# Kernel tuning notes

Hardware: AMD Instinct MI355X
Metric: run time of the kernel (lower is better)

## Reference

```python
import jax, jax.numpy as jnp
import numpy as np
from jax import lax

D_MODEL = 1024
D_STATE = 128
HEADDIM = 64
EXPAND = 2
NGROUPS = 1
CHUNK = 256
D_INNER = EXPAND * D_MODEL          # 2048
D_SSM = D_INNER                      # d_ssm defaults to d_inner
NHEADS = D_SSM // HEADDIM            # 32
CONV_DIM = D_SSM + 2 * NGROUPS * D_STATE   # 2304
D_IN_PROJ = 2 * D_INNER + 2 * NGROUPS * D_STATE + NHEADS  # 4384 -> d_mlp = 0
BATCH = 2
SEQLEN = 2048
EPS = 1e-5


def setup_inputs() -> dict:
    key = jax.random.key(0)
    ks = jax.random.split(key, 9)
    u = jax.random.normal(ks[0], (BATCH, SEQLEN, D_MODEL), jnp.float32)
    # indices into left-padded (len = SEQLEN+1) sequence; 0 selects the zero pad
    conv_indices = jax.random.randint(ks[1], (BATCH, 4 * SEQLEN), 0, SEQLEN + 1)
    W_in = jax.random.normal(ks[2], (D_IN_PROJ, D_MODEL), jnp.float32) / np.sqrt(D_MODEL).astype(np.float32)
    conv_w = jax.random.normal(ks[3], (CONV_DIM, 4), jnp.float32) * 0.2
    conv_b = jax.random.normal(ks[4], (CONV_DIM,), jnp.float32) * 0.02
    # dt_bias init exactly as the module: inverse-softplus of dt in [dt_min, dt_max]
    dt = jnp.exp(jax.random.uniform(ks[5], (NHEADS,), jnp.float32) * (np.log(0.1) - np.log(0.001)) + np.log(0.001))
    dt = jnp.clip(dt, 1e-4)
    dt_bias = dt + jnp.log(-jnp.expm1(-dt))
    A_log = jnp.log(jax.random.uniform(ks[6], (NHEADS,), jnp.float32, minval=1.0, maxval=16.0))
    D = jnp.ones((NHEADS,), jnp.float32)
    norm_w = jnp.ones((D_SSM,), jnp.float32)
    W_out = jax.random.normal(ks[7], (D_MODEL, D_INNER), jnp.float32) / np.sqrt(D_INNER).astype(np.float32)
    return dict(u=u, conv_indices=conv_indices, W_in=W_in, conv_w=conv_w, conv_b=conv_b,
                dt_bias=dt_bias, A_log=A_log, D=D, norm_w=norm_w, W_out=W_out)


def _segsum(x):
    # x: (b, c, h, cs) -> (b, c, h, cs, cs); out[..., t, s] = sum_{k=s+1..t} x[..., k]
    cs = x.shape[-1]
    cx = jnp.cumsum(x, axis=-1)
    diff = cx[..., :, None] - cx[..., None, :]
    mask = jnp.tril(jnp.ones((cs, cs), dtype=bool))
    return jnp.where(mask, diff, -jnp.inf)


def _ssd(x, dt, A, Bh, Ch, D):
    # Mamba2 SSD chunked scan. x:(b,l,h,p), dt:(b,l,h), A:(h,), Bh/Ch:(b,l,h,n), D:(h,)
    b, l, h, p = x.shape
    n = Bh.shape[-1]
    c = l // CHUNK
    xr = x.reshape(b, c, CHUNK, h, p)
    dtr = dt.reshape(b, c, CHUNK, h)
    Br = Bh.reshape(b, c, CHUNK, h, n)
    Cr = Ch.reshape(b, c, CHUNK, h, n)
    dA = dtr * A                                 # (b,c,cs,h)
    Acum = jnp.cumsum(dA, axis=2)                # (b,c,cs,h)
    Lm = jnp.exp(_segsum(jnp.transpose(dA, (0, 1, 3, 2))))  # (b,c,h,cs,cs)
    dtx = xr * dtr[..., None]                    # dt-weighted inputs
    # intra-chunk (diagonal blocks)
    Yd = jnp.einsum('bcthn,bcshn,bchts,bcshp->bcthp', Cr, Br, Lm, dtx)
    # per-chunk final states
    decay_states = jnp.exp(Acum[:, :, -1:, :] - Acum)        # (b,c,cs,h)
    states = jnp.einsum('bcshn,bcsh,bcshp->bchpn', Br, decay_states, dtx)
    chunk_decay = jnp.exp(Acum[:, :, -1, :])     # (b,c,h)
    def step(h_prev, inp):
        dec, st = inp
        return h_prev * dec[..., None, None] + st, h_prev
    init = jnp.zeros((b, h, p, n), x.dtype)
    _, prev = lax.scan(step, init, (jnp.moveaxis(chunk_decay, 1, 0), jnp.moveaxis(states, 1, 0)))
    prev = jnp.moveaxis(prev, 0, 1)              # (b,c,h,p,n): state entering each chunk
    # inter-chunk (off-diagonal) contribution
    Yoff = jnp.einsum('bcthn,bchpn,bcth->bcthp', Cr, prev, jnp.exp(Acum))
    Y = Yd + Yoff + D[None, None, None, :, None] * xr
    return Y.reshape(b, l, h, p)


def reference(u, conv_indices, W_in, conv_w, conv_b, dt_bias, A_log, D, norm_w, W_out):
    b, l, _ = u.shape
    zxbcdt = u @ W_in.T                          # (b,l,4384); d_mlp == 0
    z, xBC, dt_raw = jnp.split(zxbcdt, [D_SSM, D_SSM + CONV_DIM], axis=-1)
    # tree conv: left-pad seq by 1, gather 4 tree positions per output step, depthwise conv k=4 stride=4
    xc = jnp.transpose(xBC, (0, 2, 1))           # (b, conv_dim, l)
    xp = jnp.pad(xc, ((0, 0), (0, 0), (1, 0)))
    idx = jnp.broadcast_to(conv_indices[:, None, :], (b, CONV_DIM, 4 * l))
    g = jnp.take_along_axis(xp, idx, axis=2).reshape(b, CONV_DIM, l, 4)
    conv = jnp.einsum('bclk,ck->bcl', g, conv_w) + conv_b[None, :, None]
    xBC = jax.nn.silu(jnp.transpose(conv, (0, 2, 1)))  # (b,l,conv_dim)
    x, Bm, Cm = jnp.split(xBC, [D_SSM, D_SSM + NGROUPS * D_STATE], axis=-1)
    x = x.reshape(b, l, NHEADS, HEADDIM)
    hpg = NHEADS // NGROUPS
    Bh = jnp.repeat(Bm.reshape(b, l, NGROUPS, D_STATE), hpg, axis=2)
    Ch = jnp.repeat(Cm.reshape(b, l, NGROUPS, D_STATE), hpg, axis=2)
    dt = jax.nn.softplus(dt_raw + dt_bias)       # dt_softplus=True, default dt_limit
    A = -jnp.exp(A_log.astype(jnp.float32))
    y = _ssd(x, dt, A, Bh, Ch, D).reshape(b, l, D_SSM)
    # RMSNormGated, norm_before_gate=False, group_size = d_ssm (ngroups=1)
    yz = y * jax.nn.silu(z)
    var = jnp.mean(jnp.square(yz), axis=-1, keepdims=True)
    y = yz * lax.rsqrt(var + EPS) * norm_w
    return y @ W_out.T
```

## Files before the change

### kernel.cpp

```cpp
#include <hip/hip_runtime.h>

#define BB 2
#define LL 2048
#define DMODEL 1024
#define DSSM 2048
#define NH 32
#define HD 64
#define DST 128
#define CONVD 2304
#define DPROJ 4384
#define CS 64
#define NC 32
#define BLTOT (BB*LL)

typedef short v8s __attribute__((ext_vector_type(8)));
typedef float v4f __attribute__((ext_vector_type(4)));

__device__ __forceinline__ float b2f(unsigned short h) {
  union { unsigned int u; float f; } v; v.u = ((unsigned int)h) << 16; return v.f;
}
__device__ __forceinline__ unsigned short f2b(float f) {
  union { float f; unsigned int u; } v; v.f = f;
  unsigned int u = v.u;
  return (unsigned short)((u + 0x7fffu + ((u >> 16) & 1u)) >> 16);
}
__device__ __forceinline__ v4f mfma16(v8s a, v8s b, v4f c) {
  return __builtin_amdgcn_mfma_f32_16x16x32_bf16(a, b, c, 0, 0, 0);
}
__device__ __forceinline__ void gl_lds16(const unsigned short* g, unsigned short* l) {
  __builtin_amdgcn_global_load_lds(
      (const __attribute__((address_space(1))) void*)(g),
      (__attribute__((address_space(3))) void*)(l), 16, 0, 0);
}

__global__ __launch_bounds__(256) void cvt3_kernel(
    const float* __restrict__ a, unsigned short* __restrict__ oa, int na4,
    const float* __restrict__ b, unsigned short* __restrict__ ob, int nb4,
    const float* __restrict__ c, unsigned short* __restrict__ oc, int nc4)
{
  int i = blockIdx.x * 256 + threadIdx.x;
  const float* src; unsigned short* dst; int j;
  if (i < na4) { src = a; dst = oa; j = i; }
  else if (i < na4 + nb4) { src = b; dst = ob; j = i - na4; }
  else if (i < na4 + nb4 + nc4) { src = c; dst = oc; j = i - na4 - nb4; }
  else return;
  float4 v = ((const float4*)src)[j];
  ushort4 o;
  o.x = f2b(v.x); o.y = f2b(v.y); o.z = f2b(v.z); o.w = f2b(v.w);
  ((ushort4*)dst)[j] = o;
}

template<int TN, int OUT_BF16, int DBUF>
__global__ __launch_bounds__(256) void gemm_bt(
    const unsigned short* __restrict__ A, const unsigned short* __restrict__ Bt,
    void* __restrict__ Cout, int M, int N, int K, int ldc)
{
  constexpr int NT = TN / 32;
  constexpr int NB = DBUF ? 2 : 1;
  const int bm = blockIdx.x, bn = blockIdx.y;
  const int tid = threadIdx.x;
  const int wave = tid >> 6, lane = tid & 63;
  const int wm = wave & 1, wn = wave >> 1;
  const int q = lane >> 4, lr = lane & 15;

  __shared__ __align__(16) unsigned short As[NB][128 * 64];
  __shared__ __align__(16) unsigned short Bs[NB][TN * 64];

  v4f acc[4][NT];
#pragma unroll
  for (int i = 0; i < 4; i++)
#pragma unroll
    for (int j = 0; j < NT; j++) acc[i][j] = v4f{0.f, 0.f, 0.f, 0.f};

  const int lrow = lane >> 3;
  const int gchunk = (lane & 7) ^ lrow;

#define STAGE_TILE(bufi, k0) do {                                              \
    _Pragma("unroll")                                                          \
    for (int it = 0; it < 4; ++it) {                                           \
      int r = wave * 32 + it * 8 + lrow;                                       \
      gl_lds16(A + (size_t)(bm * 128 + r) * K + (k0) + gchunk * 8,             \
               &As[bufi][(wave * 32 + it * 8) * 64]);                          \
    }                                                                          \
    _Pragma("unroll")                                                          \
    for (int it = 0; it < TN / 32; ++it) {                                     \
      int rloc = wave * (TN / 4) + it * 8;                                     \
      int rb = bn * TN + rloc + lrow; if (rb >= N) rb = N - 1;                 \
      gl_lds16(Bt + (size_t)rb * K + (k0) + gchunk * 8, &Bs[bufi][rloc * 64]); \
    }                                                                          \
  } while (0)

#define COMPUTE_TILE(bufi) do {                                                \
    const unsigned short* __restrict__ Ab = As[bufi];                          \
    const unsigned short* __restrict__ Bb = Bs[bufi];                          \
    _Pragma("unroll")                                                          \
    for (int ks = 0; ks < 64; ks += 32) {                                      \
      const int c0 = (ks >> 3) + q;                                            \
      v8s af[4], bf[NT];                                                       \
      _Pragma("unroll")                                                        \
      for (int mt = 0; mt < 4; ++mt) {                                         \
        int r = wm * 64 + mt * 16 + lr;                                        \
        af[mt] = *(const v8s*)&Ab[r * 64 + ((c0 ^ (r & 7)) << 3)];             \
      }                                                                        \
      _Pragma("unroll")                                                        \
      for (int nt = 0; nt < NT; ++nt) {                                        \
        int r = wn * (TN / 2) + nt * 16 + lr;                                  \
        bf[nt] = *(const v8s*)&Bb[r * 64 + ((c0 ^ (r & 7)) << 3)];             \
      }                                                                        \
      _Pragma("unroll")                                                        \
      for (int mt = 0; mt < 4; ++mt)                                           \
        _Pragma("unroll")                                                      \
        for (int nt = 0; nt < NT; ++nt)                                        \
          acc[mt][nt] = mfma16(af[mt], bf[nt], acc[mt][nt]);                   \
    }                                                                          \
  } while (0)

#define WAIT_BARRIER() do {                                                    \
    __builtin_amdgcn_sched_barrier(0);                                         \
    asm volatile("s_waitcnt vmcnt(0) lgkmcnt(0)\ns_barrier" ::: "memory");     \
  } while (0)

  if constexpr (DBUF == 0) {
    for (int k0 = 0; k0 < K; k0 += 64) {
      __syncthreads();
      STAGE_TILE(0, k0);
      __syncthreads();
      COMPUTE_TILE(0);
    }
  } else {
    const int nkt = K >> 6;
    STAGE_TILE(0, 0);
    WAIT_BARRIER();
    for (int kt = 0; kt < nkt; ++kt) {
      const int cb = kt & 1;
      if (kt + 1 < nkt) STAGE_TILE(cb ^ 1, (kt + 1) << 6);
      COMPUTE_TILE(cb);
      if (kt + 1 < nkt) WAIT_BARRIER();
    }
  }
#undef STAGE_TILE
#undef COMPUTE_TILE
#undef WAIT_BARRIER

#pragma unroll
  for (int mt = 0; mt < 4; ++mt) {
#pragma unroll
    for (int nt = 0; nt < NT; ++nt) {
      int row = bm * 128 + wm * 64 + mt * 16 + q * 4;
      int col = bn * TN + wn * (TN / 2) + nt * 16 + lr;
      if (col < N) {
#pragma unroll
        for (int r = 0; r < 4; ++r) {
          float v = acc[mt][nt][r];
          if (OUT_BF16) ((unsigned short*)Cout)[(size_t)(row + r) * ldc + col] = f2b(v);
          else          ((float*)Cout)[(size_t)(row + r) * ldc + col] = v;
        }
      }
    }
  }
}

__global__ __launch_bounds__(256) void convBC_kernel(
    const unsigned short* __restrict__ C1, const int* __restrict__ cidx,
    const float* __restrict__ convw, const float* __restrict__ convb,
    const float* __restrict__ dtbias,
    unsigned short* __restrict__ Bg16, unsigned short* __restrict__ Cg16,
    unsigned short* __restrict__ BgT16, float* __restrict__ dtb)
{
  int bl0 = blockIdx.x * 16;
  int b = bl0 >> 11;
  int tid = threadIdx.x;
  __shared__ int idxs[64];
  if (tid < 64) {
    int tk = tid >> 2, k = tid & 3;
    idxs[tid] = cidx[b * (4 * LL) + (((bl0 + tk) & 2047) * 4) + k];
  }
  __syncthreads();
  const float4* cw4 = (const float4*)convw;
  int quad = tid & 63;
  int relc = DSSM + quad * 4;
  float4 w0 = cw4[relc], w1 = cw4[relc + 1], w2 = cw4[relc + 2], w3 = cw4[relc + 3];
  float4 cb = *(const float4*)(convb + relc);
  int tk0 = (tid >> 6) * 4;
  int cc = relc - DSSM;
  unsigned short btc[4][4];
#pragma unroll
  for (int tt = 0; tt < 4; ++tt) {
    int tk = tk0 + tt;
    int bl = bl0 + tk;
    ushort4 rv[4];
#pragma unroll
    for (int k = 0; k < 4; ++k) {
      int iv = idxs[tk * 4 + k];
      rv[k] = (iv > 0) ? *(const ushort4*)(C1 + (size_t)(b * LL + iv - 1) * DPROJ + DSSM + relc)
                       : make_ushort4(0, 0, 0, 0);
    }
    float a0 = cb.x + b2f(rv[0].x) * w0.x + b2f(rv[1].x) * w0.y + b2f(rv[2].x) * w0.z + b2f(rv[3].x) * w0.w;
    float a1 = cb.y + b2f(rv[0].y) * w1.x + b2f(rv[1].y) * w1.y + b2f(rv[2].y) * w1.z + b2f(rv[3].y) * w1.w;
    float a2 = cb.z + b2f(rv[0].z) * w2.x + b2f(rv[1].z) * w2.y + b2f(rv[2].z) * w2.z + b2f(rv[3].z) * w2.w;
    float a3 = cb.w + b2f(rv[0].w) * w3.x + b2f(rv[1].w) * w3.y + b2f(rv[2].w) * w3.z + b2f(rv[3].w) * w3.w;
    ushort4 o;
    o.x = f2b(a0 / (1.f + __expf(-a0)));
    o.y = f2b(a1 / (1.f + __expf(-a1)));
    o.z = f2b(a2 / (1.f + __expf(-a2)));
    o.w = f2b(a3 / (1.f + __expf(-a3)));
    if (cc < DST) {
      *(ushort4*)(Bg16 + (size_t)bl * DST + cc) = o;
      btc[0][tt] = o.x; btc[1][tt] = o.y; btc[2][tt] = o.z; btc[3][tt] = o.w;
    } else {
      *(ushort4*)(Cg16 + (size_t)bl * DST + (cc - DST)) = o;
    }
  }
  if (cc < DST) {
#pragma unroll
    for (int c = 0; c < 4; ++c)
      *(ushort4*)(BgT16 + (size_t)(cc + c) * BLTOT + bl0 + tk0) =
          make_ushort4(btc[c][0], btc[c][1], btc[c][2], btc[c][3]);
  }
  for (int u = tid; u < 16 * NH; u += 256) {
    int tk = u >> 5, hh = u & 31;
    int bl = bl0 + tk;
    float raw = b2f(C1[(size_t)bl * DPROJ + DSSM + CONVD + hh]) + dtbias[hh];
    float dtv = (raw > 20.f) ? raw : log1pf(__expf(raw));
    dtb[(size_t)bl * NH + hh] = dtv;
  }
}

__global__ __launch_bounds__(256) void d1_intra(
    const unsigned short* __restrict__ C1, const int* __restrict__ cidx,
    const float* __restrict__ convw, const float* __restrict__ convb,
    const unsigned short* __restrict__ Bg16,
    const unsigned short* __restrict__ Cg16,
    const unsigned short* __restrict__ BgT16, const float* __restrict__ dtb,
    const float* __restrict__ A_log, const float* __restrict__ Dp,
    unsigned short* __restrict__ y16, unsigned short* __restrict__ statesb,
    float* __restrict__ cdb, float* __restrict__ acumb)
{
  int gid = blockIdx.x;
  int h = gid & 31, ci = (gid >> 5) & 31, b = gid >> 10;
  int tid = threadIdx.x, wave = tid >> 6, lane = tid & 63, q = lane >> 4, lr = lane & 15;

  __shared__ __align__(16) unsigned short BnG[CS * 136];
  __shared__ __align__(16) unsigned short BTw[DST * 72];
  __shared__ __align__(16) unsigned short xT[HD * 72];
  __shared__ float dt_s[CS], ac_s[CS], dec_s[CS];
  __shared__ int idxs[CS * 4];
  __shared__ float wls[HD * 4];
  __shared__ float bls[HD];

  const size_t blbase = (size_t)b * LL + ci * CS;
  const size_t chbase = (size_t)(b * NC + ci) * NH + h;
  float Ah = -__expf(A_log[h]);

  if (wave == 0) {
    float d = dtb[(blbase + lane) * NH + h];
    float a = d * Ah;
#pragma unroll
    for (int off = 1; off < 64; off <<= 1) {
      float u = __shfl_up(a, off, 64);
      if (lane >= off) a += u;
    }
    float tot = __shfl(a, 63, 64);
    dt_s[lane] = d;
    ac_s[lane] = a;
    dec_s[lane] = __expf(tot - a);
    acumb[chbase * CS + lane] = a;
    if (lane == 0) cdb[chbase] = __expf(tot);
  }

#pragma unroll
  for (int g = 0; g < 8; ++g) {
    int f = g * 256 + tid;
    int s = f >> 5, c4 = (f & 31) * 4;
    *(ushort4*)&BnG[s * 136 + c4] = *(const ushort4*)(Bg16 + (blbase + s) * DST + c4);
  }
  {
    int s = tid >> 2, k = tid & 3;
    idxs[tid] = cidx[b * (4 * LL) + (ci * CS + s) * 4 + k];
  }
  if (tid < HD) *(float4*)&wls[tid * 4] = *(const float4*)(convw + (h * HD + tid) * 4);
  if (tid < HD / 4) *(float4*)&bls[tid * 4] = *(const float4*)(convb + h * HD + tid * 4);
  __syncthreads();

#pragma unroll
  for (int g = 0; g < 8; ++g) {
    int f = g * 256 + tid;
    int n = f >> 4, s4 = (f & 15) * 4;
    ushort4 bv = *(const ushort4*)(BgT16 + (size_t)n * BLTOT + blbase + s4);
    ushort4 o;
    o.x = f2b(b2f(bv.x) * dec_s[s4 + 0] * dt_s[s4 + 0]);
    o.y = f2b(b2f(bv.y) * dec_s[s4 + 1] * dt_s[s4 + 1]);
    o.z = f2b(b2f(bv.z) * dec_s[s4 + 2] * dt_s[s4 + 2]);
    o.w = f2b(b2f(bv.w) * dec_s[s4 + 3] * dt_s[s4 + 3]);
    *(ushort4*)&BTw[n * 72 + s4] = o;
  }

  v4f accS[4];
#pragma unroll
  for (int i = 0; i < 4; i++) accS[i] = v4f{0.f, 0.f, 0.f, 0.f};
#pragma unroll
  for (int ks = 0; ks < 128; ks += 32) {
    v8s a = *(const v8s*)(Cg16 + (blbase + wave * 16 + lr) * DST + ks + q * 8);
#pragma unroll
    for (int si = 0; si < 4; ++si) {
      v8s bb = *(const v8s*)&BnG[(si * 16 + lr) * 136 + ks + q * 8];
      accS[si] = mfma16(a, bb, accS[si]);
    }
  }

#pragma unroll
  for (int g = 0; g < 4; ++g) {
    int f = g * 256 + tid;
    int s = f >> 4, p4 = (f & 15) * 4;
    ushort4 rv[4];
#pragma unroll
    for (int k = 0; k < 4; ++k) {
      int iv = idxs[s * 4 + k];
      rv[k] = (iv > 0) ? *(const ushort4*)(C1 + (size_t)(b * LL + iv - 1) * DPROJ + DSSM + h * HD + p4)
                       : make_ushort4(0, 0, 0, 0);
    }
    float4 w0 = *(const float4*)&wls[(p4 + 0) * 4];
    float4 w1 = *(const float4*)&wls[(p4 + 1) * 4];
    float4 w2 = *(const float4*)&wls[(p4 + 2) * 4];
    float4 w3 = *(const float4*)&wls[(p4 + 3) * 4];
    float a0 = bls[p4 + 0] + b2f(rv[0].x) * w0.x + b2f(rv[1].x) * w0.y + b2f(rv[2].x) * w0.z + b2f(rv[3].x) * w0.w;
    float a1 = bls[p4 + 1] + b2f(rv[0].y) * w1.x + b2f(rv[1].y) * w1.y + b2f(rv[2].y) * w1.z + b2f(rv[3].y) * w1.w;
    float a2 = bls[p4 + 2] + b2f(rv[0].z) * w2.x + b2f(rv[1].z) * w2.y + b2f(rv[2].z) * w2.z + b2f(rv[3].z) * w2.w;
    float a3 = bls[p4 + 3] + b2f(rv[0].w) * w3.x + b2f(rv[1].w) * w3.y + b2f(rv[2].w) * w3.z + b2f(rv[3].w) * w3.w;
    xT[(p4 + 0) * 72 + s] = f2b(a0 / (1.f + __expf(-a0)));
    xT[(p4 + 1) * 72 + s] = f2b(a1 / (1.f + __expf(-a1)));
    xT[(p4 + 2) * 72 + s] = f2b(a2 / (1.f + __expf(-a2)));
    xT[(p4 + 3) * 72 + s] = f2b(a3 / (1.f + __expf(-a3)));
  }
  __syncthreads();

  {
    int tbase = wave * 16 + q * 4;
#pragma unroll
    for (int si = 0; si < 4; ++si) {
      int s = si * 16 + lr;
      float ds = dt_s[s], as = ac_s[s];
#pragma unroll
      for (int r = 0; r < 4; ++r) {
        int tt = tbase + r;
        float g = 0.f;
        if (s <= tt) g = accS[si][r] * __expf(ac_s[tt] - as) * ds;
        BnG[tt * 72 + s] = f2b(g);
      }
    }
  }
  __syncthreads();

  v4f accY[4], accPT[4][2];
#pragma unroll
  for (int i = 0; i < 4; i++) {
    accY[i] = v4f{0.f,0.f,0.f,0.f};
    accPT[i][0] = v4f{0.f,0.f,0.f,0.f};
    accPT[i][1] = v4f{0.f,0.f,0.f,0.f};
  }
  int nw = wave * 32;
#pragma unroll
  for (int ks = 0; ks < 64; ks += 32) {
    v8s xf[4];
#pragma unroll
    for (int i = 0; i < 4; ++i) xf[i] = *(const v8s*)&xT[(i * 16 + lr) * 72 + ks + q * 8];
    v8s aG  = *(const v8s*)&BnG[(wave * 16 + lr) * 72 + ks + q * 8];
    v8s bw0 = *(const v8s*)&BTw[(nw + lr) * 72 + ks + q * 8];
    v8s bw1 = *(const v8s*)&BTw[(nw + 16 + lr) * 72 + ks + q * 8];
#pragma unroll
    for (int nt = 0; nt < 4; ++nt) {
      accY[nt] = mfma16(aG, xf[nt], accY[nt]);
      accPT[nt][0] = mfma16(xf[nt], bw0, accPT[nt][0]);
      accPT[nt][1] = mfma16(xf[nt], bw1, accPT[nt][1]);
    }
  }

  float Dh = Dp[h];
#pragma unroll
  for (int nt = 0; nt < 4; ++nt) {
    int p = nt * 16 + lr;
#pragma unroll
    for (int r = 0; r < 4; ++r) {
      int t = wave * 16 + q * 4 + r;
      float xv = b2f(xT[p * 72 + t]);
      y16[(blbase + t) * DSSM + h * HD + p] = f2b(accY[nt][r] + Dh * xv);
    }
  }
  size_t sbase = chbase * (DST * HD);
#pragma unroll
  for (int mt = 0; mt < 4; ++mt) {
#pragma unroll
    for (int nt = 0; nt < 2; ++nt) {
      int n = nw + nt * 16 + lr;
#pragma unroll
      for (int r = 0; r < 4; ++r) {
        int p = mt * 16 + q * 4 + r;
        statesb[sbase + (size_t)p * DST + n] = f2b(accPT[mt][nt][r]);
      }
    }
  }
}

__global__ __launch_bounds__(256) void d2_scan(
    unsigned short* __restrict__ statesb, const float* __restrict__ cdb)
{
  int g = blockIdx.x;
  int seg = g & 7, bh = g >> 3;
  int b = bh >> 5, h = bh & 31;
  int e4 = seg * 1024 + threadIdx.x * 4;
  const size_t cstride = (size_t)NH * DST * HD;
  size_t base = ((size_t)(b * NC) * NH + h) * (DST * HD) + e4;
  ushort4 st[NC];
#pragma unroll
  for (int ci = 0; ci < NC; ++ci) st[ci] = *(const ushort4*)(statesb + base + ci * cstride);
  float r0 = 0.f, r1 = 0.f, r2 = 0.f, r3 = 0.f;
#pragma unroll
  for (int ci = 0; ci < NC; ++ci) {
    float cd = cdb[(b * NC + ci) * NH + h];
    *(ushort4*)(statesb + base + ci * cstride) =
        make_ushort4(f2b(r0), f2b(r1), f2b(r2), f2b(r3));
    r0 = r0 * cd + b2f(st[ci].x);
    r1 = r1 * cd + b2f(st[ci].y);
    r2 = r2 * cd + b2f(st[ci].z);
    r3 = r3 * cd + b2f(st[ci].w);
  }
}

__global__ __launch_bounds__(256) void d3_inter(
    const unsigned short* __restrict__ Cg16,
    const unsigned short* __restrict__ statesb, const float* __restrict__ acumb,
    unsigned short* __restrict__ y16)
{
  int gid = blockIdx.x;
  int h = gid & 31, ci = (gid >> 5) & 31, b = gid >> 10;
  int tid = threadIdx.x, wave = tid >> 6, lane = tid & 63, q = lane >> 4, lr = lane & 15;
  __shared__ __align__(16) unsigned short pT[HD * 136];
  __shared__ __align__(16) float ys[CS * 68];
  __shared__ float ea[CS];
  const size_t blbase = (size_t)b * LL + ci * CS;
  const size_t chbase = (size_t)(b * NC + ci) * NH + h;
  if (tid < CS) ea[tid] = __expf(acumb[chbase * CS + tid]);
  size_t sbase = chbase * (DST * HD);
#pragma unroll
  for (int g = 0; g < 8; ++g) {
    int f = g * 256 + tid;
    int p = f >> 5, c4 = (f & 31) * 4;
    *(ushort4*)&pT[p * 136 + c4] = *(const ushort4*)(statesb + sbase + (size_t)p * DST + c4);
  }
  __syncthreads();
  v4f acc[4];
#pragma unroll
  for (int i = 0; i < 4; i++) acc[i] = v4f{0.f, 0.f, 0.f, 0.f};
#pragma unroll
  for (int ks = 0; ks < 128; ks += 32) {
    v8s a = *(const v8s*)(Cg16 + (blbase + wave * 16 + lr) * DST + ks + q * 8);
#pragma unroll
    for (int nt = 0; nt < 4; ++nt) {
      v8s bb = *(const v8s*)&pT[(nt * 16 + lr) * 136 + ks + q * 8];
      acc[nt] = mfma16(a, bb, acc[nt]);
    }
  }
#pragma unroll
  for (int nt = 0; nt < 4; ++nt) {
#pragma unroll
    for (int r = 0; r < 4; ++r)
      ys[(wave * 16 + q * 4 + r) * 68 + nt * 16 + lr] = acc[nt][r];
  }
  __syncthreads();
#pragma unroll
  for (int it = 0; it < 2; ++it) {
    int unit = it * 256 + tid;
    int t = unit >> 3, p8 = (unit & 7) * 8;
    float ea_t = ea[t];
    size_t off = (blbase + t) * DSSM + h * HD + p8;
    uint4 yv = *(const uint4*)(y16 + off);
    float4 o0 = *(const float4*)&ys[t * 68 + p8];
    float4 o1 = *(const float4*)&ys[t * 68 + p8 + 4];
    const unsigned int* yu = (const unsigned int*)&yv;
    float oo[8] = {o0.x, o0.y, o0.z, o0.w, o1.x, o1.y, o1.z, o1.w};
    unsigned int ro[4];
#pragma unroll
    for (int d = 0; d < 4; ++d) {
      unsigned short y0 = (unsigned short)(yu[d] & 0xffffu), y1 = (unsigned short)(yu[d] >> 16);
      float v0 = b2f(y0) + ea_t * oo[d * 2 + 0];
      float v1 = b2f(y1) + ea_t * oo[d * 2 + 1];
      ro[d] = (unsigned int)f2b(v0) | ((unsigned int)f2b(v1) << 16);
    }
    *(uint4*)(y16 + off) = make_uint4(ro[0], ro[1], ro[2], ro[3]);
  }
}

__global__ __launch_bounds__(256) void norm_kernel(
    const unsigned short* __restrict__ y16, const unsigned short* __restrict__ C1,
    const float* __restrict__ normw, unsigned short* __restrict__ yzn)
{
  int bl = blockIdx.x;
  int tid = threadIdx.x;
  int wave = tid >> 6, lane = tid & 63;
  int c8 = tid * 8;
  uint4 yv = *(const uint4*)(y16 + (size_t)bl * DSSM + c8);
  uint4 zv = *(const uint4*)(C1 + (size_t)bl * DPROJ + c8);
  const unsigned int* yu = (const unsigned int*)&yv;
  const unsigned int* zu = (const unsigned int*)&zv;
  float vals[8];
  float ss = 0.f;
#pragma unroll
  for (int d = 0; d < 4; ++d) {
    unsigned short y0 = (unsigned short)(yu[d] & 0xffffu), y1 = (unsigned short)(yu[d] >> 16);
    unsigned short z0 = (unsigned short)(zu[d] & 0xffffu), z1 = (unsigned short)(zu[d] >> 16);
    float zf0 = b2f(z0), zf1 = b2f(z1);
    float v0 = b2f(y0) * (zf0 / (1.f + __expf(-zf0)));
    float v1 = b2f(y1) * (zf1 / (1.f + __expf(-zf1)));
    vals[d * 2] = v0; vals[d * 2 + 1] = v1;
    ss += v0 * v0 + v1 * v1;
  }
#pragma unroll
  for (int off = 32; off > 0; off >>= 1) ss += __shfl_down(ss, off);
  __shared__ float red[4];
  if (lane == 0) red[wave] = ss;
  __syncthreads();
  float tot = red[0] + red[1] + red[2] + red[3];
  float scale = rsqrtf(tot * (1.f / 2048.f) + 1e-5f);
  float4 w0 = *(const float4*)(normw + c8);
  float4 w1 = *(const float4*)(normw + c8 + 4);
  float ws[8] = {w0.x, w0.y, w0.z, w0.w, w1.x, w1.y, w1.z, w1.w};
  unsigned int ro[4];
#pragma unroll
  for (int d = 0; d < 4; ++d) {
    unsigned short r0 = f2b(vals[d * 2] * scale * ws[d * 2]);
    unsigned short r1 = f2b(vals[d * 2 + 1] * scale * ws[d * 2 + 1]);
    ro[d] = (unsigned int)r0 | ((unsigned int)r1 << 16);
  }
  *(uint4*)(yzn + (size_t)bl * DSSM + c8) = make_uint4(ro[0], ro[1], ro[2], ro[3]);
}

extern "C" void kernel_launch(void* const* d_in, const int* in_sizes, int n_in,
                              void* d_out, int out_size, void* d_ws, size_t ws_size,
                              hipStream_t stream) {
  const float* u      = (const float*)d_in[0];
  const int*   cidx   = (const int*)d_in[1];
  const float* W_in   = (const float*)d_in[2];
  const float* convw  = (const float*)d_in[3];
  const float* convb  = (const float*)d_in[4];
  const float* dtbias = (const float*)d_in[5];
  const float* A_log  = (const float*)d_in[6];
  const float* Dp     = (const float*)d_in[7];
  const float* normw  = (const float*)d_in[8];
  const float* W_out  = (const float*)d_in[9];

  char* w = (char*)d_ws;
  size_t off = 0;
  auto alloc = [&](size_t bytes) { char* p = w + off; off += (bytes + 255) & ~(size_t)255; return p; };
  unsigned short* u16     = (unsigned short*)alloc((size_t)BLTOT * DMODEL * 2);
  unsigned short* Win16   = (unsigned short*)alloc((size_t)DPROJ * DMODEL * 2);
  unsigned short* Wout16  = (unsigned short*)alloc((size_t)DMODEL * DSSM * 2);
  unsigned short* C1      = (unsigned short*)alloc((size_t)BLTOT * DPROJ * 2);
  unsigned short* Bg16    = (unsigned short*)alloc((size_t)BLTOT * DST * 2);
  unsigned short* Cg16    = (unsigned short*)alloc((size_t)BLTOT * DST * 2);
  unsigned short* BgT16   = (unsigned short*)alloc((size_t)DST * BLTOT * 2);
  float*          dtb     = (float*)alloc((size_t)BLTOT * NH * 4);
  float*          acumb   = (float*)alloc((size_t)BB * NC * NH * CS * 4);
  unsigned short* y16     = (unsigned short*)alloc((size_t)BLTOT * DSSM * 2);
  unsigned short* statesb = (unsigned short*)alloc((size_t)BB * NC * NH * DST * HD * 2);
  float*          cdb     = (float*)alloc((size_t)BB * NC * NH * 4);
  unsigned short* yzn     = (unsigned short*)alloc((size_t)BLTOT * DSSM * 2);

  const int na4 = BLTOT * DMODEL / 4, nb4 = DPROJ * DMODEL / 4, nc4 = DMODEL * DSSM / 4;
  cvt3_kernel<<<(na4 + nb4 + nc4 + 255) / 256, 256, 0, stream>>>(
      u, u16, na4, W_in, Win16, nb4, W_out, Wout16, nc4);

  gemm_bt<128, 1, 0><<<dim3(BLTOT / 128, (DPROJ + 127) / 128), 256, 0, stream>>>(
      u16, Win16, C1, BLTOT, DPROJ, DMODEL, DPROJ);
  convBC_kernel<<<BLTOT / 16, 256, 0, stream>>>(C1, cidx, convw, convb, dtbias,
                                                Bg16, Cg16, BgT16, dtb);
  d1_intra<<<BB * NC * NH, 256, 0, stream>>>(C1, cidx, convw, convb, Bg16, Cg16, BgT16,
                                             dtb, A_log, Dp, y16, statesb, cdb, acumb);
  d2_scan<<<BB * NH * 8, 256, 0, stream>>>(statesb, cdb);
  d3_inter<<<BB * NC * NH, 256, 0, stream>>>(Cg16, statesb, acumb, y16);
  norm_kernel<<<BLTOT, 256, 0, stream>>>(y16, C1, normw, yzn);
  gemm_bt<64, 0, 1><<<dim3(BLTOT / 128, DMODEL / 64), 256, 0, stream>>>(
      yzn, Wout16, (float*)d_out, BLTOT, DMODEL, DSSM, DMODEL);
}
```

Baseline: 254.7 us.

## Precompute head-independent C·B^T chunk matrix once per chunk in separate kernel

The C·B^T score matrix for each chunk does not depend on the head, because ngroups is 1, yet it was recomputed by all 32 head blocks in d1_intra. A new d0_S kernel computes it once per (batch, chunk) and writes it to global memory in fp32, and d1_intra reads it instead of loading B into LDS and running the MFMA loop. This removes redundant matrix-core work and the B staging, and shrinks LDS use. In exchange it adds a kernel launch with only 64 blocks and global fp32 reads of a 64x64 matrix per block. It also drops one __syncthreads; that appears safe because the S values now come from global memory rather than shared memory.

```diff
diff --git a/kernel.cpp b/kernel.cpp
--- a/kernel.cpp
+++ b/kernel.cpp
@@ -226,12 +226,46 @@
   }
 }
 
+__global__ __launch_bounds__(256) void d0_S(
+    const unsigned short* __restrict__ Bg16, const unsigned short* __restrict__ Cg16,
+    float* __restrict__ Sg)
+{
+  int gid = blockIdx.x;
+  int tid = threadIdx.x, wave = tid >> 6, lane = tid & 63, q = lane >> 4, lr = lane & 15;
+  __shared__ __align__(16) unsigned short Bn[CS * 136];
+  const size_t blbase = (size_t)(gid >> 5) * LL + (gid & 31) * CS;
+#pragma unroll
+  for (int g = 0; g < 8; ++g) {
+    int f = g * 256 + tid;
+    int s = f >> 5, c4 = (f & 31) * 4;
+    *(ushort4*)&Bn[s * 136 + c4] = *(const ushort4*)(Bg16 + (blbase + s) * DST + c4);
+  }
+  __syncthreads();
+  v4f accS[4];
+#pragma unroll
+  for (int i = 0; i < 4; i++) accS[i] = v4f{0.f, 0.f, 0.f, 0.f};
+#pragma unroll
+  for (int ks = 0; ks < 128; ks += 32) {
+    v8s a = *(const v8s*)(Cg16 + (blbase + wave * 16 + lr) * DST + ks + q * 8);
+#pragma unroll
+    for (int si = 0; si < 4; ++si) {
+      v8s bb = *(const v8s*)&Bn[(si * 16 + lr) * 136 + ks + q * 8];
+      accS[si] = mfma16(a, bb, accS[si]);
+    }
+  }
+  float* So = Sg + (size_t)gid * (CS * CS);
+#pragma unroll
+  for (int si = 0; si < 4; ++si)
+#pragma unroll
+    for (int r = 0; r < 4; ++r)
+      So[(wave * 16 + q * 4 + r) * CS + si * 16 + lr] = accS[si][r];
+}
+
 __global__ __launch_bounds__(256) void d1_intra(
     const unsigned short* __restrict__ C1, const int* __restrict__ cidx,
     const float* __restrict__ convw, const float* __restrict__ convb,
-    const unsigned short* __restrict__ Bg16,
-    const unsigned short* __restrict__ Cg16,
-    const unsigned short* __restrict__ BgT16, const float* __restrict__ dtb,
+    const unsigned short* __restrict__ BgT16, const float* __restrict__ Sg,
+    const float* __restrict__ dtb,
     const float* __restrict__ A_log, const float* __restrict__ Dp,
     unsigned short* __restrict__ y16, unsigned short* __restrict__ statesb,
     float* __restrict__ cdb, float* __restrict__ acumb)
@@ -240,7 +274,7 @@
   int h = gid & 31, ci = (gid >> 5) & 31, b = gid >> 10;
   int tid = threadIdx.x, wave = tid >> 6, lane = tid & 63, q = lane >> 4, lr = lane & 15;
 
-  __shared__ __align__(16) unsigned short BnG[CS * 136];
+  __shared__ __align__(16) unsigned short G[CS * 72];
   __shared__ __align__(16) unsigned short BTw[DST * 72];
   __shared__ __align__(16) unsigned short xT[HD * 72];
   __shared__ float dt_s[CS], ac_s[CS], dec_s[CS];
@@ -266,13 +300,6 @@
     dec_s[lane] = __expf(tot - a);
     acumb[chbase * CS + lane] = a;
     if (lane == 0) cdb[chbase] = __expf(tot);
-  }
-
-#pragma unroll
-  for (int g = 0; g < 8; ++g) {
-    int f = g * 256 + tid;
-    int s = f >> 5, c4 = (f & 31) * 4;
-    *(ushort4*)&BnG[s * 136 + c4] = *(const ushort4*)(Bg16 + (blbase + s) * DST + c4);
   }
   {
     int s = tid >> 2, k = tid & 3;
@@ -293,19 +320,6 @@
     o.z = f2b(b2f(bv.z) * dec_s[s4 + 2] * dt_s[s4 + 2]);
     o.w = f2b(b2f(bv.w) * dec_s[s4 + 3] * dt_s[s4 + 3]);
     *(ushort4*)&BTw[n * 72 + s4] = o;
-  }
-
-  v4f accS[4];
-#pragma unroll
-  for (int i = 0; i < 4; i++) accS[i] = v4f{0.f, 0.f, 0.f, 0.f};
-#pragma unroll
-  for (int ks = 0; ks < 128; ks += 32) {
-    v8s a = *(const v8s*)(Cg16 + (blbase + wave * 16 + lr) * DST + ks + q * 8);
-#pragma unroll
-    for (int si = 0; si < 4; ++si) {
-      v8s bb = *(const v8s*)&BnG[(si * 16 + lr) * 136 + ks + q * 8];
-      accS[si] = mfma16(a, bb, accS[si]);
-    }
   }
 
 #pragma unroll
@@ -332,9 +346,9 @@
     xT[(p4 + 2) * 72 + s] = f2b(a2 / (1.f + __expf(-a2)));
     xT[(p4 + 3) * 72 + s] = f2b(a3 / (1.f + __expf(-a3)));
   }
-  __syncthreads();
 
   {
+    const float* Sc = Sg + (size_t)(b * NC + ci) * (CS * CS);
     int tbase = wave * 16 + q * 4;
 #pragma unroll
     for (int si = 0; si < 4; ++si) {
@@ -344,8 +358,8 @@
       for (int r = 0; r < 4; ++r) {
         int tt = tbase + r;
         float g = 0.f;
-        if (s <= tt) g = accS[si][r] * __expf(ac_s[tt] - as) * ds;
-        BnG[tt * 72 + s] = f2b(g);
+        if (s <= tt) g = Sc[tt * CS + s] * __expf(ac_s[tt] - as) * ds;
+        G[tt * 72 + s] = f2b(g);
       }
     }
   }
@@ -364,7 +378,7 @@
     v8s xf[4];
 #pragma unroll
     for (int i = 0; i < 4; ++i) xf[i] = *(const v8s*)&xT[(i * 16 + lr) * 72 + ks + q * 8];
-    v8s aG  = *(const v8s*)&BnG[(wave * 16 + lr) * 72 + ks + q * 8];
+    v8s aG  = *(const v8s*)&G[(wave * 16 + lr) * 72 + ks + q * 8];
     v8s bw0 = *(const v8s*)&BTw[(nw + lr) * 72 + ks + q * 8];
     v8s bw1 = *(const v8s*)&BTw[(nw + 16 + lr) * 72 + ks + q * 8];
 #pragma unroll
@@ -558,6 +572,7 @@
   unsigned short* Bg16    = (unsigned short*)alloc((size_t)BLTOT * DST * 2);
   unsigned short* Cg16    = (unsigned short*)alloc((size_t)BLTOT * DST * 2);
   unsigned short* BgT16   = (unsigned short*)alloc((size_t)DST * BLTOT * 2);
+  float*          Sg      = (float*)alloc((size_t)BB * NC * CS * CS * 4);
   float*          dtb     = (float*)alloc((size_t)BLTOT * NH * 4);
   float*          acumb   = (float*)alloc((size_t)BB * NC * NH * CS * 4);
   unsigned short* y16     = (unsigned short*)alloc((size_t)BLTOT * DSSM * 2);
@@ -573,7 +588,8 @@
       u16, Win16, C1, BLTOT, DPROJ, DMODEL, DPROJ);
   convBC_kernel<<<BLTOT / 16, 256, 0, stream>>>(C1, cidx, convw, convb, dtbias,
                                                 Bg16, Cg16, BgT16, dtb);
-  d1_intra<<<BB * NC * NH, 256, 0, stream>>>(C1, cidx, convw, convb, Bg16, Cg16, BgT16,
+  d0_S<<<BB * NC, 256, 0, stream>>>(Bg16, Cg16, Sg);
+  d1_intra<<<BB * NC * NH, 256, 0, stream>>>(C1, cidx, convw, convb, BgT16, Sg,
                                              dtb, A_log, Dp, y16, statesb, cdb, acumb);
   d2_scan<<<BB * NH * 8, 256, 0, stream>>>(statesb, cdb);
   d3_inter<<<BB * NC * NH, 256, 0, stream>>>(Cg16, statesb, acumb, y16);
```

After: 254.5 us, median of 2. Within noise of the previous version (-0.1%).
